# Kernel optimization log

Hardware: AMD Instinct MI355X
Metric: run time of the kernel (lower is better)

## Reference

```python
import jax, jax.numpy as jnp
import numpy as np
import math

B, H, L, D = 2, 16, 2048, 64
THRESHOLD = 1e-5
IS_GREATER = True


def setup_inputs() -> dict:
    key = jax.random.key(0)
    kq, kk, kv = jax.random.split(key, 3)
    q = jax.random.normal(kq, (B, H, L, D), dtype=jnp.float32)
    k = jax.random.normal(kk, (B, H, L, D), dtype=jnp.float32)
    v = jax.random.normal(kv, (B, H, L, D), dtype=jnp.float32)
    return {"q": q, "k": k, "v": v}


def reference(q, k, v):
    d_tensor = q.shape[-1]
    # scaled dot-product scores: [B,H,L,L]
    score = jnp.einsum("bhqd,bhkd->bhqk", q, k) / math.sqrt(d_tensor)
    score = jax.nn.softmax(score, axis=-1)
    # column means over the query (row) axis: [B,H,L]
    col_means = jnp.mean(score, axis=2)
    if IS_GREATER:
        cols_to_keep = col_means > THRESHOLD
    else:
        cols_to_keep = col_means < THRESHOLD
    # zero out dropped columns (no renormalization, matching the original)
    score = score * cols_to_keep[:, :, None, :].astype(score.dtype)
    out = jnp.einsum("bhqk,bhkd->bhqd", score, v)
    return (out, score)
```

## Files before the change

kernel.cpp:

```cpp
#include <hip/hip_runtime.h>


#define L_ 2048
#define D_ 64
#define BH_ 32
#define NKT 32
#define QT 64

typedef __attribute__((ext_vector_type(8))) short bf16x8;
typedef __attribute__((ext_vector_type(4))) float f32x4;

__device__ __forceinline__ unsigned short f2bf(float f) {
  unsigned u = __builtin_bit_cast(unsigned, f);
  u = (u + 0x7FFFu + ((u >> 16) & 1u)) >> 16;
  return (unsigned short)u;
}
__device__ __forceinline__ float bf2f(unsigned short h) {
  unsigned u = ((unsigned)h) << 16;
  return __builtin_bit_cast(float, u);
}

__global__ void prep(const float* __restrict__ k, const float* __restrict__ v,
                     unsigned short* __restrict__ wkf, unsigned short* __restrict__ wvf) {
  __shared__ unsigned short t_[64][65];
  const int bid = blockIdx.x, tid = threadIdx.x;

  const float* ks = k + (size_t)bid * 64 * D_;
  unsigned short* kd = wkf + (size_t)bid * 4096;
#pragma unroll
  for (int it = 0; it < 2; ++it) {
    int e8 = it * 256 + tid;
    int r = e8 >> 3;
    int c0 = (e8 & 7) * 8;
    float4 f0 = *reinterpret_cast<const float4*>(ks + r * D_ + c0);
    float4 f1 = *reinterpret_cast<const float4*>(ks + r * D_ + c0 + 4);
    int t = r >> 4, lc = r & 15, h = c0 >> 5, lg = (c0 & 31) >> 3;
    unsigned short* p = kd + (t * 2 + h) * 512 + lg * 128 + lc * 8;
    ushort4 u0{f2bf(f0.x), f2bf(f0.y), f2bf(f0.z), f2bf(f0.w)};
    ushort4 u1{f2bf(f1.x), f2bf(f1.y), f2bf(f1.z), f2bf(f1.w)};
    *reinterpret_cast<ushort4*>(p) = u0;
    *reinterpret_cast<ushort4*>(p + 4) = u1;
  }

  const float* vs = v + (size_t)bid * 64 * D_;
#pragma unroll
  for (int it = 0; it < 4; ++it) {
    int e4 = tid + it * 256;
    int r = e4 >> 4, c = (e4 & 15) << 2;
    float4 f = *reinterpret_cast<const float4*>(vs + r * D_ + c);
    t_[r][c + 0] = f2bf(f.x);
    t_[r][c + 1] = f2bf(f.y);
    t_[r][c + 2] = f2bf(f.z);
    t_[r][c + 3] = f2bf(f.w);
  }
  __syncthreads();
  unsigned short* vd = wvf + (size_t)bid * 4096;
#pragma unroll
  for (int it = 0; it < 2; ++it) {
    int e8 = it * 256 + tid;
    int d = e8 >> 3;
    int k0 = (e8 & 7) * 8;
    int t = d >> 4, lc = d & 15, h = k0 >> 5, lg = (k0 & 31) >> 3;
    ushort4 u0{t_[k0 + 0][d], t_[k0 + 1][d], t_[k0 + 2][d], t_[k0 + 3][d]};
    ushort4 u1{t_[k0 + 4][d], t_[k0 + 5][d], t_[k0 + 6][d], t_[k0 + 7][d]};
    unsigned short* p = vd + (t * 2 + h) * 512 + lg * 128 + lc * 8;
    *reinterpret_cast<ushort4*>(p) = u0;
    *reinterpret_cast<ushort4*>(p + 4) = u1;
  }
}

__launch_bounds__(256, 4)
__global__ void attn_main(const float* __restrict__ qf,
                          const unsigned short* __restrict__ wkf,
                          const unsigned short* __restrict__ wvf,
                          float* __restrict__ outp,
                          float* __restrict__ score,
                          float* __restrict__ colsum) {
  __shared__ unsigned short ps[4][1024];
  __shared__ float cs_lds[2048];

  const int tid = threadIdx.x;
  const int w = tid >> 6, lane = tid & 63;
  const int lg = lane >> 4, lc = lane & 15;

  const int bid = (blockIdx.x & 7) * 128 + (blockIdx.x >> 3);
  const int bh = bid >> 5;
  const int qt = bid & 31;

  for (int i = tid; i < 2048; i += 256) cs_lds[i] = 0.0f;

  const float* qg = qf + ((size_t)bh * L_ + (size_t)qt * QT + w * 16) * D_;
  bf16x8 aq[2];
#pragma unroll
  for (int h = 0; h < 2; ++h) {
    const float* r = qg + lc * D_ + h * 32 + lg * 8;
    float4 f0 = *reinterpret_cast<const float4*>(r);
    float4 f1 = *reinterpret_cast<const float4*>(r + 4);
    bf16x8 a;
    a[0] = (short)f2bf(f0.x * 0.125f); a[1] = (short)f2bf(f0.y * 0.125f);
    a[2] = (short)f2bf(f0.z * 0.125f); a[3] = (short)f2bf(f0.w * 0.125f);
    a[4] = (short)f2bf(f1.x * 0.125f); a[5] = (short)f2bf(f1.y * 0.125f);
    a[6] = (short)f2bf(f1.z * 0.125f); a[7] = (short)f2bf(f1.w * 0.125f);
    aq[h] = a;
  }

  __syncthreads();

  const unsigned short* kg = wkf + (size_t)bh * NKT * 4096 + lg * 128 + lc * 8;
  const unsigned short* vg = wvf + (size_t)bh * NKT * 4096 + lg * 128 + lc * 8;

  float lp[4] = {0.f, 0.f, 0.f, 0.f};

#pragma unroll 2
  for (int kt = 0; kt < NKT; ++kt) {
    const unsigned short* kb = kg + kt * 4096;
    f32x4 s[4];
#pragma unroll
    for (int t = 0; t < 4; ++t) s[t] = f32x4{0.f, 0.f, 0.f, 0.f};
#pragma unroll
    for (int t = 0; t < 4; ++t) {
      bf16x8 b0 = *reinterpret_cast<const bf16x8*>(kb + (t * 2 + 0) * 512);
      bf16x8 b1 = *reinterpret_cast<const bf16x8*>(kb + (t * 2 + 1) * 512);
      s[t] = __builtin_amdgcn_mfma_f32_16x16x32_bf16(aq[0], b0, s[t], 0, 0, 0);
      s[t] = __builtin_amdgcn_mfma_f32_16x16x32_bf16(aq[1], b1, s[t], 0, 0, 0);
    }
#pragma unroll
    for (int t = 0; t < 4; ++t)
#pragma unroll
      for (int r = 0; r < 4; ++r) lp[r] += __expf(s[t][r]);
  }

  float linv[4];
#pragma unroll
  for (int r = 0; r < 4; ++r) {
    float v = lp[r];
    v += __shfl_xor(v, 1);
    v += __shfl_xor(v, 2);
    v += __shfl_xor(v, 4);
    v += __shfl_xor(v, 8);
    linv[r] = 1.0f / v;
  }

  f32x4 o[4];
#pragma unroll
  for (int dt = 0; dt < 4; ++dt) o[dt] = f32x4{0.f, 0.f, 0.f, 0.f};

  float* scoreW = score + ((size_t)bh * L_ + (size_t)qt * QT + w * 16) * L_;
  char* pw = (char*)ps[w];

#pragma unroll 1
  for (int kt = 0; kt < NKT; ++kt) {
    const unsigned short* kb = kg + kt * 4096;
    f32x4 s[4];
#pragma unroll
    for (int t = 0; t < 4; ++t) s[t] = f32x4{0.f, 0.f, 0.f, 0.f};
#pragma unroll
    for (int t = 0; t < 4; ++t) {
      bf16x8 b0 = *reinterpret_cast<const bf16x8*>(kb + (t * 2 + 0) * 512);
      bf16x8 b1 = *reinterpret_cast<const bf16x8*>(kb + (t * 2 + 1) * 512);
      s[t] = __builtin_amdgcn_mfma_f32_16x16x32_bf16(aq[0], b0, s[t], 0, 0, 0);
      s[t] = __builtin_amdgcn_mfma_f32_16x16x32_bf16(aq[1], b1, s[t], 0, 0, 0);
    }

    float ct[4] = {0.f, 0.f, 0.f, 0.f};
#pragma unroll
    for (int t = 0; t < 4; ++t)
#pragma unroll
      for (int r = 0; r < 4; ++r) {
        float p = __expf(s[t][r]) * linv[r];
        ct[t] += p;
        int prow = lg * 4 + r;
        unsigned off = ((unsigned)(prow * 128 + (t * 16 + lc) * 2)) ^ (((unsigned)(prow & 7)) << 4);
        *reinterpret_cast<unsigned short*>(pw + off) = f2bf(p);
      }

#pragma unroll
    for (int t = 0; t < 4; ++t) {
      float c = ct[t];
      c += __shfl_xor(c, 16);
      c += __shfl_xor(c, 32);
      if (lane < 16) atomicAdd(&cs_lds[kt * 64 + t * 16 + lane], c);
    }

#pragma unroll
    for (int kk = 0; kk < 2; ++kk) {
      unsigned o0 = ((unsigned)(lc * 128 + kk * 64 + lg * 16)) ^ (((unsigned)(lc & 7)) << 4);
      bf16x8 pa = *reinterpret_cast<const bf16x8*>(pw + o0);
      const unsigned short* vb = vg + kt * 4096 + kk * 512;
#pragma unroll
      for (int dt = 0; dt < 4; ++dt) {
        bf16x8 bv = *reinterpret_cast<const bf16x8*>(vb + dt * 1024);
        o[dt] = __builtin_amdgcn_mfma_f32_16x16x32_bf16(pa, bv, o[dt], 0, 0, 0);
      }
    }

#pragma unroll
    for (int rnd = 0; rnd < 2; ++rnd) {
      int prow = rnd * 8 + (lane >> 3);
      int colc = (lane & 7) * 8;
      unsigned off = ((unsigned)(prow * 128 + colc * 2)) ^ (((unsigned)(prow & 7)) << 4);
      bf16x8 p8 = *reinterpret_cast<const bf16x8*>(pw + off);
      f32x4 f0, f1;
      f0[0] = bf2f((unsigned short)p8[0]); f0[1] = bf2f((unsigned short)p8[1]);
      f0[2] = bf2f((unsigned short)p8[2]); f0[3] = bf2f((unsigned short)p8[3]);
      f1[0] = bf2f((unsigned short)p8[4]); f1[1] = bf2f((unsigned short)p8[5]);
      f1[2] = bf2f((unsigned short)p8[6]); f1[3] = bf2f((unsigned short)p8[7]);
      float* sg = scoreW + (size_t)prow * L_ + kt * 64 + colc;
      __builtin_nontemporal_store(f0, reinterpret_cast<f32x4*>(sg));
      __builtin_nontemporal_store(f1, reinterpret_cast<f32x4*>(sg + 4));
    }
  }

  float* og = outp + ((size_t)bh * L_ + (size_t)qt * QT + w * 16) * D_;
#pragma unroll
  for (int dt = 0; dt < 4; ++dt)
#pragma unroll
    for (int r = 0; r < 4; ++r)
      __builtin_nontemporal_store(o[dt][r], og + (lg * 4 + r) * D_ + dt * 16 + lc);

  __syncthreads();
  for (int i = tid; i < L_; i += 256) atomicAdd(&colsum[bh * L_ + i], cs_lds[i]);
}

__global__ void mask_fix(float* __restrict__ outp, float* __restrict__ score,
                         const float* __restrict__ colsum, const float* __restrict__ v) {
  __shared__ int drop_list[2048];
  __shared__ int ndrop;
  int bh = blockIdx.x;
  if (threadIdx.x == 0) ndrop = 0;
  __syncthreads();
  for (int c = threadIdx.x; c < L_; c += 256) {
    float mean = colsum[bh * L_ + c] * (1.0f / 2048.0f);
    if (!(mean > 1e-5f)) {
      int idx = atomicAdd(&ndrop, 1);
      drop_list[idx] = c;
    }
  }
  __syncthreads();
  int nd = ndrop;
  if (nd == 0) return;
  float* sc = score + (size_t)bh * L_ * L_;
  float* ob = outp + (size_t)bh * L_ * D_;
  const float* vb = v + (size_t)bh * L_ * D_;
  for (int i = 0; i < nd; ++i) {
    int k = drop_list[i];
    for (int idx = threadIdx.x; idx < L_ * D_; idx += 256) {
      int q = idx >> 6, d = idx & 63;
      ob[q * D_ + d] -= sc[(size_t)q * L_ + k] * vb[k * D_ + d];
    }
    __syncthreads();
  }
  for (int i = 0; i < nd; ++i) {
    int k = drop_list[i];
    for (int q = threadIdx.x; q < L_; q += 256) sc[(size_t)q * L_ + k] = 0.0f;
  }
}

extern "C" void kernel_launch(void* const* d_in, const int* in_sizes, int n_in,
                              void* d_out, int out_size, void* d_ws, size_t ws_size,
                              hipStream_t stream) {
  const float* q = (const float*)d_in[0];
  const float* k = (const float*)d_in[1];
  const float* v = (const float*)d_in[2];
  float* outp = (float*)d_out;
  float* score = outp + (size_t)BH_ * L_ * D_;

  unsigned short* wkf = (unsigned short*)d_ws;
  unsigned short* wvf = wkf + (size_t)BH_ * L_ * D_;
  float* colsum = (float*)(wvf + (size_t)BH_ * L_ * D_);

  (void)hipMemsetAsync(colsum, 0, BH_ * L_ * sizeof(float), stream);
  prep<<<BH_ * NKT, 256, 0, stream>>>(k, v, wkf, wvf);
  attn_main<<<1024, 256, 0, stream>>>(q, wkf, wvf, outp, score, colsum);
  mask_fix<<<BH_, 256, 0, stream>>>(outp, score, colsum, v);
}
```

Baseline: 209.1 us.

## Process two query tiles per block, fusing tile-B row-sum pass into tile-A loop

Each block now handles two 64-row query tiles, so the grid shrinks to 512 blocks. The row-sum (softmax denominator) pass for the second tile is folded into the first tile's main loop, sharing the K fragment loads, which removes one separate QK^T sweep per pair. The colsum memset is moved into the prep kernel, and the column-sum LDS atomics are staggered per wave to spread bank contention. Occupancy is lowered to 2 blocks per CU and register pressure rises.

```diff
diff --git a/kernel.cpp b/kernel.cpp
--- a/kernel.cpp
+++ b/kernel.cpp
@@ -5,7 +5,6 @@
 #define D_ 64
 #define BH_ 32
 #define NKT 32
-#define QT 64
 
 typedef __attribute__((ext_vector_type(8))) short bf16x8;
 typedef __attribute__((ext_vector_type(4))) float f32x4;
@@ -21,9 +20,15 @@
 }
 
 __global__ void prep(const float* __restrict__ k, const float* __restrict__ v,
-                     unsigned short* __restrict__ wkf, unsigned short* __restrict__ wvf) {
+                     unsigned short* __restrict__ wkf, unsigned short* __restrict__ wvf,
+                     float* __restrict__ colsum) {
   __shared__ unsigned short t_[64][65];
   const int bid = blockIdx.x, tid = threadIdx.x;
+
+  if (bid < 64) {
+    float* cz = colsum + bid * 1024;
+    for (int i = tid; i < 1024; i += 256) cz[i] = 0.0f;
+  }
 
   const float* ks = k + (size_t)bid * 64 * D_;
   unsigned short* kd = wkf + (size_t)bid * 4096;
@@ -69,7 +74,7 @@
   }
 }
 
-__launch_bounds__(256, 4)
+__launch_bounds__(256, 2)
 __global__ void attn_main(const float* __restrict__ qf,
                           const unsigned short* __restrict__ wkf,
                           const unsigned short* __restrict__ wvf,
@@ -83,25 +88,34 @@
   const int w = tid >> 6, lane = tid & 63;
   const int lg = lane >> 4, lc = lane & 15;
 
-  const int bid = (blockIdx.x & 7) * 128 + (blockIdx.x >> 3);
-  const int bh = bid >> 5;
-  const int qt = bid & 31;
+  const int bid = (blockIdx.x & 7) * 64 + (blockIdx.x >> 3);
+  const int bh = bid >> 4;
+  const int qp = bid & 15;
+  const int rowA = qp * 128 + w * 16;
+  const int rowB = rowA + 64;
 
   for (int i = tid; i < 2048; i += 256) cs_lds[i] = 0.0f;
 
-  const float* qg = qf + ((size_t)bh * L_ + (size_t)qt * QT + w * 16) * D_;
-  bf16x8 aq[2];
+  bf16x8 aqA[2], aqB[2];
 #pragma unroll
   for (int h = 0; h < 2; ++h) {
-    const float* r = qg + lc * D_ + h * 32 + lg * 8;
-    float4 f0 = *reinterpret_cast<const float4*>(r);
-    float4 f1 = *reinterpret_cast<const float4*>(r + 4);
-    bf16x8 a;
-    a[0] = (short)f2bf(f0.x * 0.125f); a[1] = (short)f2bf(f0.y * 0.125f);
-    a[2] = (short)f2bf(f0.z * 0.125f); a[3] = (short)f2bf(f0.w * 0.125f);
-    a[4] = (short)f2bf(f1.x * 0.125f); a[5] = (short)f2bf(f1.y * 0.125f);
-    a[6] = (short)f2bf(f1.z * 0.125f); a[7] = (short)f2bf(f1.w * 0.125f);
-    aq[h] = a;
+    const float* rA = qf + ((size_t)bh * L_ + rowA + lc) * D_ + h * 32 + lg * 8;
+    const float* rB = qf + ((size_t)bh * L_ + rowB + lc) * D_ + h * 32 + lg * 8;
+    float4 a0 = *reinterpret_cast<const float4*>(rA);
+    float4 a1 = *reinterpret_cast<const float4*>(rA + 4);
+    float4 b0 = *reinterpret_cast<const float4*>(rB);
+    float4 b1 = *reinterpret_cast<const float4*>(rB + 4);
+    bf16x8 a, b;
+    a[0] = (short)f2bf(a0.x * 0.125f); a[1] = (short)f2bf(a0.y * 0.125f);
+    a[2] = (short)f2bf(a0.z * 0.125f); a[3] = (short)f2bf(a0.w * 0.125f);
+    a[4] = (short)f2bf(a1.x * 0.125f); a[5] = (short)f2bf(a1.y * 0.125f);
+    a[6] = (short)f2bf(a1.z * 0.125f); a[7] = (short)f2bf(a1.w * 0.125f);
+    b[0] = (short)f2bf(b0.x * 0.125f); b[1] = (short)f2bf(b0.y * 0.125f);
+    b[2] = (short)f2bf(b0.z * 0.125f); b[3] = (short)f2bf(b0.w * 0.125f);
+    b[4] = (short)f2bf(b1.x * 0.125f); b[5] = (short)f2bf(b1.y * 0.125f);
+    b[6] = (short)f2bf(b1.z * 0.125f); b[7] = (short)f2bf(b1.w * 0.125f);
+    aqA[h] = a;
+    aqB[h] = b;
   }
 
   __syncthreads();
@@ -109,8 +123,7 @@
   const unsigned short* kg = wkf + (size_t)bh * NKT * 4096 + lg * 128 + lc * 8;
   const unsigned short* vg = wvf + (size_t)bh * NKT * 4096 + lg * 128 + lc * 8;
 
-  float lp[4] = {0.f, 0.f, 0.f, 0.f};
-
+  float lpA[4] = {0.f, 0.f, 0.f, 0.f};
 #pragma unroll 2
   for (int kt = 0; kt < NKT; ++kt) {
     const unsigned short* kb = kg + kt * 4096;
@@ -121,45 +134,55 @@
     for (int t = 0; t < 4; ++t) {
       bf16x8 b0 = *reinterpret_cast<const bf16x8*>(kb + (t * 2 + 0) * 512);
       bf16x8 b1 = *reinterpret_cast<const bf16x8*>(kb + (t * 2 + 1) * 512);
-      s[t] = __builtin_amdgcn_mfma_f32_16x16x32_bf16(aq[0], b0, s[t], 0, 0, 0);
-      s[t] = __builtin_amdgcn_mfma_f32_16x16x32_bf16(aq[1], b1, s[t], 0, 0, 0);
+      s[t] = __builtin_amdgcn_mfma_f32_16x16x32_bf16(aqA[0], b0, s[t], 0, 0, 0);
+      s[t] = __builtin_amdgcn_mfma_f32_16x16x32_bf16(aqA[1], b1, s[t], 0, 0, 0);
     }
 #pragma unroll
     for (int t = 0; t < 4; ++t)
 #pragma unroll
-      for (int r = 0; r < 4; ++r) lp[r] += __expf(s[t][r]);
-  }
-
-  float linv[4];
+      for (int r = 0; r < 4; ++r) lpA[r] += __expf(s[t][r]);
+  }
+
+  float linvA[4];
 #pragma unroll
   for (int r = 0; r < 4; ++r) {
-    float v = lp[r];
+    float v = lpA[r];
     v += __shfl_xor(v, 1);
     v += __shfl_xor(v, 2);
     v += __shfl_xor(v, 4);
     v += __shfl_xor(v, 8);
-    linv[r] = 1.0f / v;
-  }
-
+    linvA[r] = 1.0f / v;
+  }
+
+  float lpB[4] = {0.f, 0.f, 0.f, 0.f};
   f32x4 o[4];
 #pragma unroll
   for (int dt = 0; dt < 4; ++dt) o[dt] = f32x4{0.f, 0.f, 0.f, 0.f};
 
-  float* scoreW = score + ((size_t)bh * L_ + (size_t)qt * QT + w * 16) * L_;
+  float* scoreA = score + ((size_t)bh * L_ + rowA) * L_;
   char* pw = (char*)ps[w];
 
 #pragma unroll 1
   for (int kt = 0; kt < NKT; ++kt) {
     const unsigned short* kb = kg + kt * 4096;
-    f32x4 s[4];
-#pragma unroll
-    for (int t = 0; t < 4; ++t) s[t] = f32x4{0.f, 0.f, 0.f, 0.f};
-#pragma unroll
-    for (int t = 0; t < 4; ++t) {
-      bf16x8 b0 = *reinterpret_cast<const bf16x8*>(kb + (t * 2 + 0) * 512);
-      bf16x8 b1 = *reinterpret_cast<const bf16x8*>(kb + (t * 2 + 1) * 512);
-      s[t] = __builtin_amdgcn_mfma_f32_16x16x32_bf16(aq[0], b0, s[t], 0, 0, 0);
-      s[t] = __builtin_amdgcn_mfma_f32_16x16x32_bf16(aq[1], b1, s[t], 0, 0, 0);
+    bf16x8 kf[8];
+#pragma unroll
+    for (int t = 0; t < 4; ++t) {
+      kf[2 * t + 0] = *reinterpret_cast<const bf16x8*>(kb + (t * 2 + 0) * 512);
+      kf[2 * t + 1] = *reinterpret_cast<const bf16x8*>(kb + (t * 2 + 1) * 512);
+    }
+    f32x4 sA[4], sB[4];
+#pragma unroll
+    for (int t = 0; t < 4; ++t) {
+      sA[t] = f32x4{0.f, 0.f, 0.f, 0.f};
+      sB[t] = f32x4{0.f, 0.f, 0.f, 0.f};
+    }
+#pragma unroll
+    for (int t = 0; t < 4; ++t) {
+      sA[t] = __builtin_amdgcn_mfma_f32_16x16x32_bf16(aqA[0], kf[2 * t + 0], sA[t], 0, 0, 0);
+      sA[t] = __builtin_amdgcn_mfma_f32_16x16x32_bf16(aqA[1], kf[2 * t + 1], sA[t], 0, 0, 0);
+      sB[t] = __builtin_amdgcn_mfma_f32_16x16x32_bf16(aqB[0], kf[2 * t + 0], sB[t], 0, 0, 0);
+      sB[t] = __builtin_amdgcn_mfma_f32_16x16x32_bf16(aqB[1], kf[2 * t + 1], sB[t], 0, 0, 0);
     }
 
     float ct[4] = {0.f, 0.f, 0.f, 0.f};
@@ -167,7 +190,7 @@
     for (int t = 0; t < 4; ++t)
 #pragma unroll
       for (int r = 0; r < 4; ++r) {
-        float p = __expf(s[t][r]) * linv[r];
+        float p = __expf(sA[t][r]) * linvA[r];
         ct[t] += p;
         int prow = lg * 4 + r;
         unsigned off = ((unsigned)(prow * 128 + (t * 16 + lc) * 2)) ^ (((unsigned)(prow & 7)) << 4);
@@ -176,10 +199,11 @@
 
 #pragma unroll
     for (int t = 0; t < 4; ++t) {
-      float c = ct[t];
+      int tt = (t + w) & 3;
+      float c = ct[tt];
       c += __shfl_xor(c, 16);
       c += __shfl_xor(c, 32);
-      if (lane < 16) atomicAdd(&cs_lds[kt * 64 + t * 16 + lane], c);
+      if (lane < 16) atomicAdd(&cs_lds[kt * 64 + tt * 16 + lane], c);
     }
 
 #pragma unroll
@@ -205,18 +229,113 @@
       f0[2] = bf2f((unsigned short)p8[2]); f0[3] = bf2f((unsigned short)p8[3]);
       f1[0] = bf2f((unsigned short)p8[4]); f1[1] = bf2f((unsigned short)p8[5]);
       f1[2] = bf2f((unsigned short)p8[6]); f1[3] = bf2f((unsigned short)p8[7]);
-      float* sg = scoreW + (size_t)prow * L_ + kt * 64 + colc;
+      float* sg = scoreA + (size_t)prow * L_ + kt * 64 + colc;
       __builtin_nontemporal_store(f0, reinterpret_cast<f32x4*>(sg));
       __builtin_nontemporal_store(f1, reinterpret_cast<f32x4*>(sg + 4));
     }
-  }
-
-  float* og = outp + ((size_t)bh * L_ + (size_t)qt * QT + w * 16) * D_;
-#pragma unroll
-  for (int dt = 0; dt < 4; ++dt)
-#pragma unroll
-    for (int r = 0; r < 4; ++r)
-      __builtin_nontemporal_store(o[dt][r], og + (lg * 4 + r) * D_ + dt * 16 + lc);
+
+#pragma unroll
+    for (int t = 0; t < 4; ++t)
+#pragma unroll
+      for (int r = 0; r < 4; ++r) lpB[r] += __expf(sB[t][r]);
+  }
+
+  {
+    float* og = outp + ((size_t)bh * L_ + rowA) * D_;
+#pragma unroll
+    for (int dt = 0; dt < 4; ++dt)
+#pragma unroll
+      for (int r = 0; r < 4; ++r)
+        __builtin_nontemporal_store(o[dt][r], og + (lg * 4 + r) * D_ + dt * 16 + lc);
+  }
+
+  float linvB[4];
+#pragma unroll
+  for (int r = 0; r < 4; ++r) {
+    float v = lpB[r];
+    v += __shfl_xor(v, 1);
+    v += __shfl_xor(v, 2);
+    v += __shfl_xor(v, 4);
+    v += __shfl_xor(v, 8);
+    linvB[r] = 1.0f / v;
+  }
+
+#pragma unroll
+  for (int dt = 0; dt < 4; ++dt) o[dt] = f32x4{0.f, 0.f, 0.f, 0.f};
+  float* scoreB = score + ((size_t)bh * L_ + rowB) * L_;
+
+#pragma unroll 1
+  for (int kt = 0; kt < NKT; ++kt) {
+    const unsigned short* kb = kg + kt * 4096;
+    f32x4 sB[4];
+#pragma unroll
+    for (int t = 0; t < 4; ++t) sB[t] = f32x4{0.f, 0.f, 0.f, 0.f};
+#pragma unroll
+    for (int t = 0; t < 4; ++t) {
+      bf16x8 b0 = *reinterpret_cast<const bf16x8*>(kb + (t * 2 + 0) * 512);
+      bf16x8 b1 = *reinterpret_cast<const bf16x8*>(kb + (t * 2 + 1) * 512);
+      sB[t] = __builtin_amdgcn_mfma_f32_16x16x32_bf16(aqB[0], b0, sB[t], 0, 0, 0);
+      sB[t] = __builtin_amdgcn_mfma_f32_16x16x32_bf16(aqB[1], b1, sB[t], 0, 0, 0);
+    }
+
+    float ct[4] = {0.f, 0.f, 0.f, 0.f};
+#pragma unroll
+    for (int t = 0; t < 4; ++t)
+#pragma unroll
+      for (int r = 0; r < 4; ++r) {
+        float p = __expf(sB[t][r]) * linvB[r];
+        ct[t] += p;
+        int prow = lg * 4 + r;
+        unsigned off = ((unsigned)(prow * 128 + (t * 16 + lc) * 2)) ^ (((unsigned)(prow & 7)) << 4);
+        *reinterpret_cast<unsigned short*>(pw + off) = f2bf(p);
+      }
+
+#pragma unroll
+    for (int t = 0; t < 4; ++t) {
+      int tt = (t + w) & 3;
+      float c = ct[tt];
+      c += __shfl_xor(c, 16);
+      c += __shfl_xor(c, 32);
+      if (lane < 16) atomicAdd(&cs_lds[kt * 64 + tt * 16 + lane], c);
+    }
+
+#pragma unroll
+    for (int kk = 0; kk < 2; ++kk) {
+      unsigned o0 = ((unsigned)(lc * 128 + kk * 64 + lg * 16)) ^ (((unsigned)(lc & 7)) << 4);
+      bf16x8 pa = *reinterpret_cast<const bf16x8*>(pw + o0);
+      const unsigned short* vb = vg + kt * 4096 + kk * 512;
+#pragma unroll
+      for (int dt = 0; dt < 4; ++dt) {
+        bf16x8 bv = *reinterpret_cast<const bf16x8*>(vb + dt * 1024);
+        o[dt] = __builtin_amdgcn_mfma_f32_16x16x32_bf16(pa, bv, o[dt], 0, 0, 0);
+      }
+    }
+
+#pragma unroll
+    for (int rnd = 0; rnd < 2; ++rnd) {
+      int prow = rnd * 8 + (lane >> 3);
+      int colc = (lane & 7) * 8;
+      unsigned off = ((unsigned)(prow * 128 + colc * 2)) ^ (((unsigned)(prow & 7)) << 4);
+      bf16x8 p8 = *reinterpret_cast<const bf16x8*>(pw + off);
+      f32x4 f0, f1;
+      f0[0] = bf2f((unsigned short)p8[0]); f0[1] = bf2f((unsigned short)p8[1]);
+      f0[2] = bf2f((unsigned short)p8[2]); f0[3] = bf2f((unsigned short)p8[3]);
+      f1[0] = bf2f((unsigned short)p8[4]); f1[1] = bf2f((unsigned short)p8[5]);
+      f1[2] = bf2f((unsigned short)p8[6]); f1[3] = bf2f((unsigned short)p8[7]);
+      float* sg = scoreB + (size_t)prow * L_ + kt * 64 + colc;
+      __builtin_nontemporal_store(f0, reinterpret_cast<f32x4*>(sg));
+      __builtin_nontemporal_store(f1, reinterpret_cast<f32x4*>(sg + 4));
+    }
+  }
+
+  {
+    float* og = outp + ((size_t)bh * L_ + rowB) * D_;
+#pragma unroll
+    for (int dt = 0; dt < 4; ++dt)
+#pragma unroll
+      for (int r = 0; r < 4; ++r)
+        __builtin_nontemporal_store(o[dt][r], og + (lg * 4 + r) * D_ + dt * 16 + lc);
+  }
 
   __syncthreads();
   for (int i = tid; i < L_; i += 256) atomicAdd(&colsum[bh * L_ + i], cs_lds[i]);
@@ -269,8 +388,7 @@
   unsigned short* wvf = wkf + (size_t)BH_ * L_ * D_;
   float* colsum = (float*)(wvf + (size_t)BH_ * L_ * D_);
 
-  (void)hipMemsetAsync(colsum, 0, BH_ * L_ * sizeof(float), stream);
-  prep<<<BH_ * NKT, 256, 0, stream>>>(k, v, wkf, wvf);
-  attn_main<<<1024, 256, 0, stream>>>(q, wkf, wvf, outp, score, colsum);
+  prep<<<BH_ * NKT, 256, 0, stream>>>(k, v, wkf, wvf, colsum);
+  attn_main<<<512, 256, 0, stream>>>(q, wkf, wvf, outp, score, colsum);
   mask_fix<<<BH_, 256, 0, stream>>>(outp, score, colsum, v);
 }
```

Measured after the change: 220.7 us. 1.06x slower.

## Stage K tiles in LDS via async global_load_lds double buffering

Applied to the files above, without the earlier changes.

Each K tile is now loaded cooperatively into a double-buffered LDS region with global_load_lds, prefetching the next tile while the current one is used, instead of every wave reading K straight from global memory. The colsum zeroing moves into the prep kernel, which drops the separate memset. The per-wave order of the LDS column-sum atomics is rotated to reduce conflicts. This adds barriers, hand-written vmcnt waits that must match the number of outstanding loads, and 16KB more LDS, which may lower occupancy.

```diff
diff --git a/kernel.cpp b/kernel.cpp
--- a/kernel.cpp
+++ b/kernel.cpp
@@ -5,7 +5,6 @@
 #define D_ 64
 #define BH_ 32
 #define NKT 32
-#define QT 64
 
 typedef __attribute__((ext_vector_type(8))) short bf16x8;
 typedef __attribute__((ext_vector_type(4))) float f32x4;
@@ -19,11 +18,22 @@
   unsigned u = ((unsigned)h) << 16;
   return __builtin_bit_cast(float, u);
 }
+__device__ __forceinline__ void gload_lds16(const void* g, void* l) {
+  __builtin_amdgcn_global_load_lds((const __attribute__((address_space(1))) void*)g,
+                                   (__attribute__((address_space(3))) void*)l, 16, 0, 0);
+}
+#define BAR() asm volatile("s_barrier" ::: "memory")
 
 __global__ void prep(const float* __restrict__ k, const float* __restrict__ v,
-                     unsigned short* __restrict__ wkf, unsigned short* __restrict__ wvf) {
+                     unsigned short* __restrict__ wkf, unsigned short* __restrict__ wvf,
+                     float* __restrict__ colsum) {
   __shared__ unsigned short t_[64][65];
   const int bid = blockIdx.x, tid = threadIdx.x;
+
+  if (bid < 64) {
+    float* cz = colsum + bid * 1024;
+    for (int i = tid; i < 1024; i += 256) cz[i] = 0.0f;
+  }
 
   const float* ks = k + (size_t)bid * 64 * D_;
   unsigned short* kd = wkf + (size_t)bid * 4096;
@@ -76,7 +86,8 @@
                           float* __restrict__ outp,
                           float* __restrict__ score,
                           float* __restrict__ colsum) {
-  __shared__ unsigned short ps[4][1024];
+  __shared__ __align__(16) unsigned short kb[2][4096];
+  __shared__ __align__(16) unsigned short ps[4][1024];
   __shared__ float cs_lds[2048];
 
   const int tid = threadIdx.x;
@@ -89,7 +100,7 @@
 
   for (int i = tid; i < 2048; i += 256) cs_lds[i] = 0.0f;
 
-  const float* qg = qf + ((size_t)bh * L_ + (size_t)qt * QT + w * 16) * D_;
+  const float* qg = qf + ((size_t)bh * L_ + (size_t)qt * 64 + w * 16) * D_;
   bf16x8 aq[2];
 #pragma unroll
   for (int h = 0; h < 2; ++h) {
@@ -104,23 +115,39 @@
     aq[h] = a;
   }
 
-  __syncthreads();
-
-  const unsigned short* kg = wkf + (size_t)bh * NKT * 4096 + lg * 128 + lc * 8;
-  const unsigned short* vg = wvf + (size_t)bh * NKT * 4096 + lg * 128 + lc * 8;
+  const unsigned short* ktiles = wkf + (size_t)bh * NKT * 4096;
+  const unsigned short* vg = wvf + (size_t)bh * NKT * 4096 + lane * 8;
+  const int ub = w * 1024;
+
+  __syncthreads();
 
   float lp[4] = {0.f, 0.f, 0.f, 0.f};
-
-#pragma unroll 2
+  {
+    const unsigned short* g = ktiles + ub + lane * 8;
+    gload_lds16(g, &kb[0][ub]);
+    gload_lds16(g + 512, &kb[0][ub + 512]);
+  }
+  int b = 0;
+#pragma unroll 1
   for (int kt = 0; kt < NKT; ++kt) {
-    const unsigned short* kb = kg + kt * 4096;
+    if (kt + 1 < NKT) {
+      const unsigned short* g = ktiles + (kt + 1) * 4096 + ub + lane * 8;
+      gload_lds16(g, &kb[b ^ 1][ub]);
+      gload_lds16(g + 512, &kb[b ^ 1][ub + 512]);
+      asm volatile("s_waitcnt vmcnt(2)" ::: "memory");
+    } else {
+      asm volatile("s_waitcnt vmcnt(0)" ::: "memory");
+    }
+    BAR();
+
+    const unsigned short* kbl = kb[b] + lane * 8;
     f32x4 s[4];
 #pragma unroll
     for (int t = 0; t < 4; ++t) s[t] = f32x4{0.f, 0.f, 0.f, 0.f};
 #pragma unroll
     for (int t = 0; t < 4; ++t) {
-      bf16x8 b0 = *reinterpret_cast<const bf16x8*>(kb + (t * 2 + 0) * 512);
-      bf16x8 b1 = *reinterpret_cast<const bf16x8*>(kb + (t * 2 + 1) * 512);
+      bf16x8 b0 = *reinterpret_cast<const bf16x8*>(kbl + (t * 2 + 0) * 512);
+      bf16x8 b1 = *reinterpret_cast<const bf16x8*>(kbl + (t * 2 + 1) * 512);
       s[t] = __builtin_amdgcn_mfma_f32_16x16x32_bf16(aq[0], b0, s[t], 0, 0, 0);
       s[t] = __builtin_amdgcn_mfma_f32_16x16x32_bf16(aq[1], b1, s[t], 0, 0, 0);
     }
@@ -128,8 +155,17 @@
     for (int t = 0; t < 4; ++t)
 #pragma unroll
       for (int r = 0; r < 4; ++r) lp[r] += __expf(s[t][r]);
-  }
-
+
+    asm volatile("s_waitcnt lgkmcnt(0)" ::: "memory");
+    BAR();
+    b ^= 1;
+  }
+
+  {
+    const unsigned short* g = ktiles + ub + lane * 8;
+    gload_lds16(g, &kb[0][ub]);
+    gload_lds16(g + 512, &kb[0][ub + 512]);
+  }
   float linv[4];
 #pragma unroll
   for (int r = 0; r < 4; ++r) {
@@ -145,19 +181,30 @@
 #pragma unroll
   for (int dt = 0; dt < 4; ++dt) o[dt] = f32x4{0.f, 0.f, 0.f, 0.f};
 
-  float* scoreW = score + ((size_t)bh * L_ + (size_t)qt * QT + w * 16) * L_;
+  float* scoreW = score + ((size_t)bh * L_ + (size_t)qt * 64 + w * 16) * L_;
   char* pw = (char*)ps[w];
+  b = 0;
 
 #pragma unroll 1
   for (int kt = 0; kt < NKT; ++kt) {
-    const unsigned short* kb = kg + kt * 4096;
+    if (kt + 1 < NKT) {
+      const unsigned short* g = ktiles + (kt + 1) * 4096 + ub + lane * 8;
+      gload_lds16(g, &kb[b ^ 1][ub]);
+      gload_lds16(g + 512, &kb[b ^ 1][ub + 512]);
+    }
+    if (kt == 0)               asm volatile("s_waitcnt vmcnt(2)" ::: "memory");
+    else if (kt + 1 < NKT)     asm volatile("s_waitcnt vmcnt(6)" ::: "memory");
+    else                       asm volatile("s_waitcnt vmcnt(4)" ::: "memory");
+    BAR();
+
+    const unsigned short* kbl = kb[b] + lane * 8;
     f32x4 s[4];
 #pragma unroll
     for (int t = 0; t < 4; ++t) s[t] = f32x4{0.f, 0.f, 0.f, 0.f};
 #pragma unroll
     for (int t = 0; t < 4; ++t) {
-      bf16x8 b0 = *reinterpret_cast<const bf16x8*>(kb + (t * 2 + 0) * 512);
-      bf16x8 b1 = *reinterpret_cast<const bf16x8*>(kb + (t * 2 + 1) * 512);
+      bf16x8 b0 = *reinterpret_cast<const bf16x8*>(kbl + (t * 2 + 0) * 512);
+      bf16x8 b1 = *reinterpret_cast<const bf16x8*>(kbl + (t * 2 + 1) * 512);
       s[t] = __builtin_amdgcn_mfma_f32_16x16x32_bf16(aq[0], b0, s[t], 0, 0, 0);
       s[t] = __builtin_amdgcn_mfma_f32_16x16x32_bf16(aq[1], b1, s[t], 0, 0, 0);
     }
@@ -176,10 +223,11 @@
 
 #pragma unroll
     for (int t = 0; t < 4; ++t) {
-      float c = ct[t];
+      int tt = (t + w) & 3;
+      float c = ct[tt];
       c += __shfl_xor(c, 16);
       c += __shfl_xor(c, 32);
-      if (lane < 16) atomicAdd(&cs_lds[kt * 64 + t * 16 + lane], c);
+      if (lane < 16) atomicAdd(&cs_lds[kt * 64 + tt * 16 + lane], c);
     }
 
 #pragma unroll
@@ -209,9 +257,13 @@
       __builtin_nontemporal_store(f0, reinterpret_cast<f32x4*>(sg));
       __builtin_nontemporal_store(f1, reinterpret_cast<f32x4*>(sg + 4));
     }
-  }
-
-  float* og = outp + ((size_t)bh * L_ + (size_t)qt * QT + w * 16) * D_;
+
+    asm volatile("s_waitcnt lgkmcnt(0)" ::: "memory");
+    BAR();
+    b ^= 1;
+  }
+
+  float* og = outp + ((size_t)bh * L_ + (size_t)qt * 64 + w * 16) * D_;
 #pragma unroll
   for (int dt = 0; dt < 4; ++dt)
 #pragma unroll
@@ -269,8 +321,7 @@
   unsigned short* wvf = wkf + (size_t)BH_ * L_ * D_;
   float* colsum = (float*)(wvf + (size_t)BH_ * L_ * D_);
 
-  (void)hipMemsetAsync(colsum, 0, BH_ * L_ * sizeof(float), stream);
-  prep<<<BH_ * NKT, 256, 0, stream>>>(k, v, wkf, wvf);
+  prep<<<BH_ * NKT, 256, 0, stream>>>(k, v, wkf, wvf, colsum);
   attn_main<<<1024, 256, 0, stream>>>(q, wkf, wvf, outp, score, colsum);
   mask_fix<<<BH_, 256, 0, stream>>>(outp, score, colsum, v);
 }
```

Measured after the change: 211.0 us (median of 3 runs). About the same (+0.9%).

## Double-buffer P tiles, widen score row writes, stage output via LDS, fuse colsum zeroing

Applied to the files above, without the earlier changes.

Each wave now processes key tiles in pairs with two LDS P buffers, so a score row is written as 128 contiguous floats per pair instead of 64 per tile. The output tile is staged through LDS so global stores become 16-byte vectors instead of scalar stores. The colsum memset is folded into the prep kernel, which removes a separate launch, and the LDS column-sum atomics are rotated per wave to reduce bank contention. The cost is more LDS use per block and a slightly longer, more complex inner loop.

```diff
diff --git a/kernel.cpp b/kernel.cpp
--- a/kernel.cpp
+++ b/kernel.cpp
@@ -5,7 +5,6 @@
 #define D_ 64
 #define BH_ 32
 #define NKT 32
-#define QT 64
 
 typedef __attribute__((ext_vector_type(8))) short bf16x8;
 typedef __attribute__((ext_vector_type(4))) float f32x4;
@@ -21,9 +20,15 @@
 }
 
 __global__ void prep(const float* __restrict__ k, const float* __restrict__ v,
-                     unsigned short* __restrict__ wkf, unsigned short* __restrict__ wvf) {
+                     unsigned short* __restrict__ wkf, unsigned short* __restrict__ wvf,
+                     float* __restrict__ colsum) {
   __shared__ unsigned short t_[64][65];
   const int bid = blockIdx.x, tid = threadIdx.x;
+
+  if (bid < 64) {
+    float* cz = colsum + bid * 1024;
+    for (int i = tid; i < 1024; i += 256) cz[i] = 0.0f;
+  }
 
   const float* ks = k + (size_t)bid * 64 * D_;
   unsigned short* kd = wkf + (size_t)bid * 4096;
@@ -76,7 +81,7 @@
                           float* __restrict__ outp,
                           float* __restrict__ score,
                           float* __restrict__ colsum) {
-  __shared__ unsigned short ps[4][1024];
+  __shared__ __align__(16) unsigned short ps[4][2][1024];
   __shared__ float cs_lds[2048];
 
   const int tid = threadIdx.x;
@@ -89,7 +94,7 @@
 
   for (int i = tid; i < 2048; i += 256) cs_lds[i] = 0.0f;
 
-  const float* qg = qf + ((size_t)bh * L_ + (size_t)qt * QT + w * 16) * D_;
+  const float* qg = qf + ((size_t)bh * L_ + (size_t)qt * 64 + w * 16) * D_;
   bf16x8 aq[2];
 #pragma unroll
   for (int h = 0; h < 2; ++h) {
@@ -145,78 +150,96 @@
 #pragma unroll
   for (int dt = 0; dt < 4; ++dt) o[dt] = f32x4{0.f, 0.f, 0.f, 0.f};
 
-  float* scoreW = score + ((size_t)bh * L_ + (size_t)qt * QT + w * 16) * L_;
-  char* pw = (char*)ps[w];
+  float* scoreW = score + ((size_t)bh * L_ + (size_t)qt * 64 + w * 16) * L_;
 
 #pragma unroll 1
-  for (int kt = 0; kt < NKT; ++kt) {
-    const unsigned short* kb = kg + kt * 4096;
-    f32x4 s[4];
-#pragma unroll
-    for (int t = 0; t < 4; ++t) s[t] = f32x4{0.f, 0.f, 0.f, 0.f};
-#pragma unroll
-    for (int t = 0; t < 4; ++t) {
-      bf16x8 b0 = *reinterpret_cast<const bf16x8*>(kb + (t * 2 + 0) * 512);
-      bf16x8 b1 = *reinterpret_cast<const bf16x8*>(kb + (t * 2 + 1) * 512);
-      s[t] = __builtin_amdgcn_mfma_f32_16x16x32_bf16(aq[0], b0, s[t], 0, 0, 0);
-      s[t] = __builtin_amdgcn_mfma_f32_16x16x32_bf16(aq[1], b1, s[t], 0, 0, 0);
-    }
-
-    float ct[4] = {0.f, 0.f, 0.f, 0.f};
-#pragma unroll
-    for (int t = 0; t < 4; ++t)
-#pragma unroll
-      for (int r = 0; r < 4; ++r) {
-        float p = __expf(s[t][r]) * linv[r];
-        ct[t] += p;
-        int prow = lg * 4 + r;
-        unsigned off = ((unsigned)(prow * 128 + (t * 16 + lc) * 2)) ^ (((unsigned)(prow & 7)) << 4);
-        *reinterpret_cast<unsigned short*>(pw + off) = f2bf(p);
-      }
-
-#pragma unroll
-    for (int t = 0; t < 4; ++t) {
-      float c = ct[t];
-      c += __shfl_xor(c, 16);
-      c += __shfl_xor(c, 32);
-      if (lane < 16) atomicAdd(&cs_lds[kt * 64 + t * 16 + lane], c);
-    }
-
-#pragma unroll
-    for (int kk = 0; kk < 2; ++kk) {
-      unsigned o0 = ((unsigned)(lc * 128 + kk * 64 + lg * 16)) ^ (((unsigned)(lc & 7)) << 4);
-      bf16x8 pa = *reinterpret_cast<const bf16x8*>(pw + o0);
-      const unsigned short* vb = vg + kt * 4096 + kk * 512;
-#pragma unroll
-      for (int dt = 0; dt < 4; ++dt) {
-        bf16x8 bv = *reinterpret_cast<const bf16x8*>(vb + dt * 1024);
-        o[dt] = __builtin_amdgcn_mfma_f32_16x16x32_bf16(pa, bv, o[dt], 0, 0, 0);
+  for (int ktp = 0; ktp < NKT / 2; ++ktp) {
+#pragma unroll
+    for (int half = 0; half < 2; ++half) {
+      const int kt = ktp * 2 + half;
+      const unsigned short* kb = kg + kt * 4096;
+      char* pw = (char*)ps[w][half];
+
+      f32x4 s[4];
+#pragma unroll
+      for (int t = 0; t < 4; ++t) s[t] = f32x4{0.f, 0.f, 0.f, 0.f};
+#pragma unroll
+      for (int t = 0; t < 4; ++t) {
+        bf16x8 b0 = *reinterpret_cast<const bf16x8*>(kb + (t * 2 + 0) * 512);
+        bf16x8 b1 = *reinterpret_cast<const bf16x8*>(kb + (t * 2 + 1) * 512);
+        s[t] = __builtin_amdgcn_mfma_f32_16x16x32_bf16(aq[0], b0, s[t], 0, 0, 0);
+        s[t] = __builtin_amdgcn_mfma_f32_16x16x32_bf16(aq[1], b1, s[t], 0, 0, 0);
+      }
+
+      float ct[4] = {0.f, 0.f, 0.f, 0.f};
+#pragma unroll
+      for (int t = 0; t < 4; ++t)
+#pragma unroll
+        for (int r = 0; r < 4; ++r) {
+          float p = __expf(s[t][r]) * linv[r];
+          ct[t] += p;
+          int prow = lg * 4 + r;
+          unsigned off = ((unsigned)(prow * 128 + (t * 16 + lc) * 2)) ^ (((unsigned)(prow & 7)) << 4);
+          *reinterpret_cast<unsigned short*>(pw + off) = f2bf(p);
+        }
+
+#pragma unroll
+      for (int t = 0; t < 4; ++t) {
+        int tt = (t + w) & 3;
+        float c = ct[tt];
+        c += __shfl_xor(c, 16);
+        c += __shfl_xor(c, 32);
+        if (lane < 16) atomicAdd(&cs_lds[kt * 64 + tt * 16 + lane], c);
+      }
+
+#pragma unroll
+      for (int kk = 0; kk < 2; ++kk) {
+        unsigned o0 = ((unsigned)(lc * 128 + kk * 64 + lg * 16)) ^ (((unsigned)(lc & 7)) << 4);
+        bf16x8 pa = *reinterpret_cast<const bf16x8*>(pw + o0);
+        const unsigned short* vb = vg + kt * 4096 + kk * 512;
+#pragma unroll
+        for (int dt = 0; dt < 4; ++dt) {
+          bf16x8 bv = *reinterpret_cast<const bf16x8*>(vb + dt * 1024);
+          o[dt] = __builtin_amdgcn_mfma_f32_16x16x32_bf16(pa, bv, o[dt], 0, 0, 0);
+        }
       }
     }
 
 #pragma unroll
     for (int rnd = 0; rnd < 2; ++rnd) {
       int prow = rnd * 8 + (lane >> 3);
-      int colc = (lane & 7) * 8;
-      unsigned off = ((unsigned)(prow * 128 + colc * 2)) ^ (((unsigned)(prow & 7)) << 4);
-      bf16x8 p8 = *reinterpret_cast<const bf16x8*>(pw + off);
-      f32x4 f0, f1;
-      f0[0] = bf2f((unsigned short)p8[0]); f0[1] = bf2f((unsigned short)p8[1]);
-      f0[2] = bf2f((unsigned short)p8[2]); f0[3] = bf2f((unsigned short)p8[3]);
-      f1[0] = bf2f((unsigned short)p8[4]); f1[1] = bf2f((unsigned short)p8[5]);
-      f1[2] = bf2f((unsigned short)p8[6]); f1[3] = bf2f((unsigned short)p8[7]);
-      float* sg = scoreW + (size_t)prow * L_ + kt * 64 + colc;
-      __builtin_nontemporal_store(f0, reinterpret_cast<f32x4*>(sg));
-      __builtin_nontemporal_store(f1, reinterpret_cast<f32x4*>(sg + 4));
-    }
-  }
-
-  float* og = outp + ((size_t)bh * L_ + (size_t)qt * QT + w * 16) * D_;
-#pragma unroll
-  for (int dt = 0; dt < 4; ++dt)
-#pragma unroll
-    for (int r = 0; r < 4; ++r)
-      __builtin_nontemporal_store(o[dt][r], og + (lg * 4 + r) * D_ + dt * 16 + lc);
+      int j = lane & 7;
+      unsigned base = (unsigned)(prow * 128);
+      unsigned sw = ((unsigned)(prow & 7)) << 4;
+      float* rowp = scoreW + (size_t)prow * L_ + ktp * 128 + j * 4;
+#pragma unroll
+      for (int c = 0; c < 4; ++c) {
+        const char* pw = (const char*)ps[w][c >> 1];
+        unsigned off = (base + (c & 1) * 64 + j * 8) ^ sw;
+        ushort4 p4 = *reinterpret_cast<const ushort4*>(pw + off);
+        f32x4 f;
+        f[0] = bf2f(p4.x); f[1] = bf2f(p4.y); f[2] = bf2f(p4.z); f[3] = bf2f(p4.w);
+        __builtin_nontemporal_store(f, reinterpret_cast<f32x4*>(rowp + c * 32));
+      }
+    }
+  }
+
+  {
+    float* ow = reinterpret_cast<float*>(&ps[w][0][0]);
+#pragma unroll
+    for (int dt = 0; dt < 4; ++dt)
+#pragma unroll
+      for (int r = 0; r < 4; ++r)
+        ow[(lg * 4 + r) * 64 + dt * 16 + lc] = o[dt][r];
+    float* og = outp + ((size_t)bh * L_ + (size_t)qt * 64 + w * 16) * D_;
+#pragma unroll
+    for (int it = 0; it < 4; ++it) {
+      int i = it * 64 + lane;
+      int row = i >> 4, c4 = (i & 15) * 4;
+      f32x4 f = *reinterpret_cast<const f32x4*>(ow + row * 64 + c4);
+      __builtin_nontemporal_store(f, reinterpret_cast<f32x4*>(og + (size_t)row * D_ + c4));
+    }
+  }
 
   __syncthreads();
   for (int i = tid; i < L_; i += 256) atomicAdd(&colsum[bh * L_ + i], cs_lds[i]);
@@ -269,8 +292,7 @@
   unsigned short* wvf = wkf + (size_t)BH_ * L_ * D_;
   float* colsum = (float*)(wvf + (size_t)BH_ * L_ * D_);
 
-  (void)hipMemsetAsync(colsum, 0, BH_ * L_ * sizeof(float), stream);
-  prep<<<BH_ * NKT, 256, 0, stream>>>(k, v, wkf, wvf);
+  prep<<<BH_ * NKT, 256, 0, stream>>>(k, v, wkf, wvf, colsum);
   attn_main<<<1024, 256, 0, stream>>>(q, wkf, wvf, outp, score, colsum);
   mask_fix<<<BH_, 256, 0, stream>>>(outp, score, colsum, v);
 }
```

Result: faster. 170.8 us (-18.3%).
